# Optimization experiments

Hardware: AMD Instinct MI355X
Metric: run time of the kernel (lower is better)

## Reference

```python
import jax, jax.numpy as jnp
import numpy as np

B, N, C, H = 64, 4096, 128, 4
ALPHA = 0.2  # leaky_relu negative slope


def setup_inputs() -> dict:
    key = jax.random.key(0)
    k1, k2, k3, k4, k5 = jax.random.split(key, 5)
    V = jax.random.normal(k1, (B, N, C), dtype=jnp.float32)
    graph_size = jax.random.randint(k2, (B,), 1, N + 1, dtype=jnp.int32)
    # xavier_uniform-like init for weight [C, H*C] and tune_weight [1, H, C]
    lim_w = float(np.sqrt(6.0 / (C + H * C)))
    weight = jax.random.uniform(k3, (C, H * C), minval=-lim_w, maxval=lim_w, dtype=jnp.float32)
    lim_t = float(np.sqrt(6.0 / (H + C)))
    tune_weight = jax.random.uniform(k4, (1, H, C), minval=-lim_t, maxval=lim_t, dtype=jnp.float32)
    bias = jnp.full((H * C,), 0.01, dtype=jnp.float32)
    return {"V": V, "graph_size": graph_size, "weight": weight, "bias": bias, "tune_weight": tune_weight}


def reference(V, graph_size, weight, bias, tune_weight):
    # valid-node mask: node n of graph b is valid iff n < graph_size[b]
    mask = jnp.arange(N)[None, :] < graph_size[:, None]          # [B, N]
    # linear projection: [B, N, C] @ [C, H*C] + bias -> [B, N, H, C]
    Vg = (jnp.einsum('bnc,cd->bnd', V, weight) + bias).reshape(B, N, H, C)
    # attention logits per head: sum over features of tune_weight * Vg
    a = jnp.einsum('bnhc,ohc->bnh', Vg, tune_weight)             # [B, N, H]
    a = jnp.where(a >= 0, a, ALPHA * a)                          # leaky_relu
    # per-graph (segment) softmax over valid nodes
    a = jnp.where(mask[:, :, None], a, -jnp.inf)
    a = jax.nn.softmax(a, axis=1)                                # [B, N, H]
    # weighted segment sum -> [B, H, C] -> [B, H*C] (concat=True)
    out = jnp.einsum('bnhc,bnh->bhc', Vg, a)
    return out.reshape(B, H * C)
```

## Files before the change

### kernel.cpp

```cpp
#include <hip/hip_runtime.h>

#define NB 64
#define NN 4096
#define NC 128
#define NH 4
#define HC (NH * NC)
#define PSTRIDE (8 + HC)
#define NSLICE 16
#define LRELU 0.2f

__global__ __launch_bounds__(128) void k0_wt(const float* __restrict__ W,
                                             const float* __restrict__ bias,
                                             const float* __restrict__ tune,
                                             float* __restrict__ wtbt)
{
    const int bid = blockIdx.x;
    const int t = threadIdx.x;
    const float* src = (bid < NC) ? (W + (size_t)bid * HC) : bias;
    float* dst = (bid < NC) ? (wtbt + bid * NH) : (wtbt + NC * NH);
    const float4 a = reinterpret_cast<const float4*>(src)[t];
    const float4 b = reinterpret_cast<const float4*>(tune)[t];
    float p = a.x * b.x + a.y * b.y + a.z * b.z + a.w * b.w;
    #pragma unroll
    for (int off = 16; off; off >>= 1) p += __shfl_xor(p, off, 32);
    if ((t & 31) == 0) dst[t >> 5] = p;
}

__global__ __launch_bounds__(256, 4) void k1_part(const float* __restrict__ V,
                                                  const int* __restrict__ gs,
                                                  const float* __restrict__ wtbt,
                                                  float* __restrict__ part)
{
    const int slice = blockIdx.x;
    const int b = blockIdx.y;
    const int tid = threadIdx.x;
    const int hw = tid >> 5;
    const int lane = tid & 31;
    const int h = lane >> 3;
    const int j = lane & 7;
    const int w = slice * 8 + hw;
    const int gsz = gs[b];

    float wtk[16];
    #pragma unroll
    for (int u = 0; u < 16; ++u) wtk[u] = wtbt[(16 * j + u) * NH + h];
    const float bt = wtbt[HC + h];

    const int rem = gsz - w;
    const int iters = rem > 0 ? ((rem + 127) >> 7) : 0;

    float l = 0.f;
    float S[16] = {};

    const size_t STR = (size_t)128 * NC;
    const float* vp = V + ((size_t)b * NN + w) * NC + j * 16;

    float4 A0, A1, A2, A3, B0, B1, B2, B3;
    if (iters > 0) {
        A0 = reinterpret_cast<const float4*>(vp)[0];
        A1 = reinterpret_cast<const float4*>(vp)[1];
        A2 = reinterpret_cast<const float4*>(vp)[2];
        A3 = reinterpret_cast<const float4*>(vp)[3];
        const float* p1 = vp + (iters > 1 ? STR : 0);
        B0 = reinterpret_cast<const float4*>(p1)[0];
        B1 = reinterpret_cast<const float4*>(p1)[1];
        B2 = reinterpret_cast<const float4*>(p1)[2];
        B3 = reinterpret_cast<const float4*>(p1)[3];
    }
    for (int i = 0; i < iters; ++i) {
        const float* p2 = vp + (i + 2 < iters ? 2 * STR : 0);
        const float4 C0 = reinterpret_cast<const float4*>(p2)[0];
        const float4 C1 = reinterpret_cast<const float4*>(p2)[1];
        const float4 C2 = reinterpret_cast<const float4*>(p2)[2];
        const float4 C3 = reinterpret_cast<const float4*>(p2)[3];
        vp += STR;

        float a0 = A0.x * wtk[0]  + A0.y * wtk[1]  + A0.z * wtk[2]  + A0.w * wtk[3];
        float a1 = A1.x * wtk[4]  + A1.y * wtk[5]  + A1.z * wtk[6]  + A1.w * wtk[7];
        float a2 = A2.x * wtk[8]  + A2.y * wtk[9]  + A2.z * wtk[10] + A2.w * wtk[11];
        float a3 = A3.x * wtk[12] + A3.y * wtk[13] + A3.z * wtk[14] + A3.w * wtk[15];
        float lg = (a0 + a1) + (a2 + a3);
        lg += __shfl_xor(lg, 1, 32);
        lg += __shfl_xor(lg, 2, 32);
        lg += __shfl_xor(lg, 4, 32);
        float x = lg + bt;
        x = (x >= 0.f) ? x : LRELU * x;
        const float p = __expf(x);
        l += p;
        S[0]  += p * A0.x;  S[1]  += p * A0.y;  S[2]  += p * A0.z;  S[3]  += p * A0.w;
        S[4]  += p * A1.x;  S[5]  += p * A1.y;  S[6]  += p * A1.z;  S[7]  += p * A1.w;
        S[8]  += p * A2.x;  S[9]  += p * A2.y;  S[10] += p * A2.z;  S[11] += p * A2.w;
        S[12] += p * A3.x;  S[13] += p * A3.y;  S[14] += p * A3.z;  S[15] += p * A3.w;
        A0 = B0; A1 = B1; A2 = B2; A3 = B3;
        B0 = C0; B1 = C1; B2 = C2; B3 = C3;
    }

    __shared__ float llds[8][4];
    __shared__ float Sall[8][4][132];
    if (j == 0) llds[hw][h] = l;
    #pragma unroll
    for (int t = 0; t < 4; ++t) {
        float4 s4;
        s4.x = S[4 * t]; s4.y = S[4 * t + 1]; s4.z = S[4 * t + 2]; s4.w = S[4 * t + 3];
        *reinterpret_cast<float4*>(&Sall[hw][h][16 * j + 4 * t]) = s4;
    }
    __syncthreads();
    float* pb = part + (size_t)(b * NSLICE + slice) * PSTRIDE;
    if (tid < 4) {
        pb[tid] = 0.f;
        float L = 0.f;
        #pragma unroll
        for (int ww = 0; ww < 8; ++ww) L += llds[ww][tid];
        pb[4 + tid] = L;
    }
    #pragma unroll
    for (int r = 0; r < 2; ++r) {
        const int e = tid + r * 256;
        const int hh = e >> 7, k = e & 127;
        float s = 0.f;
        #pragma unroll
        for (int ww = 0; ww < 8; ++ww) s += Sall[ww][hh][k];
        pb[8 + e] = s;
    }
}

__global__ __launch_bounds__(128) void k2_out(const float* __restrict__ part,
                                              const float* __restrict__ W,
                                              const float* __restrict__ bias,
                                              float* __restrict__ out)
{
    const int b = blockIdx.x;
    const int h = blockIdx.y;
    const int tid = threadIdx.x;
    const float* pb = part + (size_t)b * NSLICE * PSTRIDE;

    __shared__ float Sn[NC];
    __shared__ float sL;
    if (tid == 0) {
        float L = 0.f;
        #pragma unroll
        for (int c = 0; c < NSLICE; ++c) L += pb[(size_t)c * PSTRIDE + 4 + h];
        sL = L;
    }
    __syncthreads();
    {
        float s = 0.f;
        #pragma unroll 4
        for (int c = 0; c < NSLICE; ++c)
            s += pb[(size_t)c * PSTRIDE + 8 + h * NC + tid];
        Sn[tid] = s / sL;
    }
    __syncthreads();
    const int d = h * NC + tid;
    float acc = 0.f;
    #pragma unroll 4
    for (int k = 0; k < NC; ++k) acc += Sn[k] * W[(size_t)k * HC + d];
    out[(size_t)b * HC + d] = acc + bias[d];
}

extern "C" void kernel_launch(void* const* d_in, const int* in_sizes, int n_in,
                              void* d_out, int out_size, void* d_ws, size_t ws_size,
                              hipStream_t stream)
{
    const float* V    = (const float*)d_in[0];
    const int*   gsz  = (const int*)d_in[1];
    const float* W    = (const float*)d_in[2];
    const float* bias = (const float*)d_in[3];
    const float* tune = (const float*)d_in[4];
    float* out  = (float*)d_out;
    float* wtbt = (float*)d_ws;
    float* part = wtbt + PSTRIDE;

    hipLaunchKernelGGL(k0_wt, dim3(NC + 1), dim3(128), 0, stream, W, bias, tune, wtbt);
    hipLaunchKernelGGL(k1_part, dim3(NSLICE, NB), dim3(256), 0, stream, V, gsz, wtbt, part);
    hipLaunchKernelGGL(k2_out, dim3(NB, NH), dim3(128), 0, stream, part, W, bias, out);
}
```

Measured before the change: 49.58 us.

## Fuse final reduction and output projection into partial kernel via last-block atomic counter

Removes the separate output kernel: each slice block writes its partials, fences, and atomically bumps a per-graph counter. The last block for a graph merges all slices, normalises and does the 128x512 projection. k0 now zeroes the counters each call. This saves a kernel launch and its dependency gap, at the cost of an atomic, fences, and a serial tail of work done by one block per graph.

Measured after the change: 180.2 us. 263% more time.

```diff
diff --git a/kernel.cpp b/kernel.cpp
--- a/kernel.cpp
+++ b/kernel.cpp
@@ -9,6 +9,7 @@
 #define NSLICE 16
 #define LRELU 0.2f
 
+
 __global__ __launch_bounds__(128) void k0_wt(const float* __restrict__ W,
                                              const float* __restrict__ bias,
                                              const float* __restrict__ tune,
@@ -16,6 +17,9 @@
 {
     const int bid = blockIdx.x;
     const int t = threadIdx.x;
+    if (bid == NC && t < 64) {
+        reinterpret_cast<int*>(wtbt + PSTRIDE)[t] = 0;
+    }
     const float* src = (bid < NC) ? (W + (size_t)bid * HC) : bias;
     float* dst = (bid < NC) ? (wtbt + bid * NH) : (wtbt + NC * NH);
     const float4 a = reinterpret_cast<const float4*>(src)[t];
@@ -26,11 +30,17 @@
     if ((t & 31) == 0) dst[t >> 5] = p;
 }
 
-__global__ __launch_bounds__(256, 4) void k1_part(const float* __restrict__ V,
-                                                  const int* __restrict__ gs,
-                                                  const float* __restrict__ wtbt,
-                                                  float* __restrict__ part)
+__global__ __launch_bounds__(256, 4) void k1_fused(const float* __restrict__ V,
+                                                   const int* __restrict__ gs,
+                                                   float* __restrict__ ws,
+                                                   const float* __restrict__ W,
+                                                   const float* __restrict__ bias,
+                                                   float* __restrict__ out)
 {
+    const float* wtbt = ws;
+    int* cnt = reinterpret_cast<int*>(ws + PSTRIDE);
+    float* part = ws + PSTRIDE + 64;
+
     const int slice = blockIdx.x;
     const int b = blockIdx.y;
     const int tid = threadIdx.x;
@@ -97,6 +107,9 @@
 
     __shared__ float llds[8][4];
     __shared__ float Sall[8][4][132];
+    __shared__ float sLh[4];
+    __shared__ float MrgSn[HC];
+    __shared__ int   sOld;
     if (j == 0) llds[hw][h] = l;
     #pragma unroll
     for (int t = 0; t < 4; ++t) {
@@ -107,7 +120,6 @@
     __syncthreads();
     float* pb = part + (size_t)(b * NSLICE + slice) * PSTRIDE;
     if (tid < 4) {
-        pb[tid] = 0.f;
         float L = 0.f;
         #pragma unroll
         for (int ww = 0; ww < 8; ++ww) L += llds[ww][tid];
@@ -122,40 +134,40 @@
         for (int ww = 0; ww < 8; ++ww) s += Sall[ww][hh][k];
         pb[8 + e] = s;
     }
-}
 
-__global__ __launch_bounds__(128) void k2_out(const float* __restrict__ part,
-                                              const float* __restrict__ W,
-                                              const float* __restrict__ bias,
-                                              float* __restrict__ out)
-{
-    const int b = blockIdx.x;
-    const int h = blockIdx.y;
-    const int tid = threadIdx.x;
-    const float* pb = part + (size_t)b * NSLICE * PSTRIDE;
+    __threadfence();
+    __syncthreads();
+    if (tid == 0) sOld = atomicAdd(&cnt[b], 1);
+    __syncthreads();
+    if (sOld != NSLICE - 1) return;
+    __threadfence();
 
-    __shared__ float Sn[NC];
-    __shared__ float sL;
-    if (tid == 0) {
+    const float* pg = part + (size_t)b * NSLICE * PSTRIDE;
+    if (tid < 4) {
         float L = 0.f;
         #pragma unroll
-        for (int c = 0; c < NSLICE; ++c) L += pb[(size_t)c * PSTRIDE + 4 + h];
-        sL = L;
+        for (int c = 0; c < NSLICE; ++c) L += pg[(size_t)c * PSTRIDE + 4 + tid];
+        sLh[tid] = L;
     }
     __syncthreads();
-    {
+    #pragma unroll
+    for (int r = 0; r < 2; ++r) {
+        const int e = tid + r * 256;
         float s = 0.f;
         #pragma unroll 4
-        for (int c = 0; c < NSLICE; ++c)
-            s += pb[(size_t)c * PSTRIDE + 8 + h * NC + tid];
-        Sn[tid] = s / sL;
+        for (int c = 0; c < NSLICE; ++c) s += pg[(size_t)c * PSTRIDE + 8 + e];
+        MrgSn[e] = s / sLh[e >> 7];
     }
     __syncthreads();
-    const int d = h * NC + tid;
-    float acc = 0.f;
-    #pragma unroll 4
-    for (int k = 0; k < NC; ++k) acc += Sn[k] * W[(size_t)k * HC + d];
-    out[(size_t)b * HC + d] = acc + bias[d];
+    #pragma unroll
+    for (int r = 0; r < 2; ++r) {
+        const int d = tid + r * 256;
+        const int hh = d >> 7;
+        float acc = 0.f;
+        #pragma unroll 4
+        for (int k = 0; k < NC; ++k) acc += MrgSn[hh * NC + k] * W[(size_t)k * HC + d];
+        out[(size_t)b * HC + d] = acc + bias[d];
+    }
 }
 
 extern "C" void kernel_launch(void* const* d_in, const int* in_sizes, int n_in,
@@ -167,11 +179,9 @@
     const float* W    = (const float*)d_in[2];
     const float* bias = (const float*)d_in[3];
     const float* tune = (const float*)d_in[4];
-    float* out  = (float*)d_out;
-    float* wtbt = (float*)d_ws;
-    float* part = wtbt + PSTRIDE;
+    float* out = (float*)d_out;
+    float* ws  = (float*)d_ws;
 
-    hipLaunchKernelGGL(k0_wt, dim3(NC + 1), dim3(128), 0, stream, W, bias, tune, wtbt);
-    hipLaunchKernelGGL(k1_part, dim3(NSLICE, NB), dim3(256), 0, stream, V, gsz, wtbt, part);
-    hipLaunchKernelGGL(k2_out, dim3(NB, NH), dim3(128), 0, stream, part, W, bias, out);
+    hipLaunchKernelGGL(k0_wt, dim3(NC + 1), dim3(128), 0, stream, W, bias, tune, ws);
+    hipLaunchKernelGGL(k1_fused, dim3(NSLICE, NB), dim3(256), 0, stream, V, gsz, ws, W, bias, out);
 }
```

## Double slices and interleave two row streams per warp; merge heads in output kernel

Applied to the files above, without the earlier changes.

Raises the number of node slices per graph so more blocks run concurrently. Each warp now processes two independent rows per iteration, one 256 rows further on, with their loads and shuffle reductions interleaved to raise memory-level parallelism. The final kernel handles all four heads in one 256-thread block per graph. The cost is more partial sums to reduce and a larger register footprint per thread.

New measurement: 66.51 us. 1.34x slower.

```diff
diff --git a/kernel.cpp b/kernel.cpp
--- a/kernel.cpp
+++ b/kernel.cpp
@@ -6,7 +6,7 @@
 #define NH 4
 #define HC (NH * NC)
 #define PSTRIDE (8 + HC)
-#define NSLICE 16
+#define NSLICE 32
 #define LRELU 0.2f
 
 __global__ __launch_bounds__(128) void k0_wt(const float* __restrict__ W,
@@ -47,52 +47,73 @@
     const float bt = wtbt[HC + h];
 
     const int rem = gsz - w;
-    const int iters = rem > 0 ? ((rem + 127) >> 7) : 0;
+    const int iters = rem > 0 ? ((rem + 255) >> 8) : 0;
+    const int npair = (iters + 1) >> 1;
 
     float l = 0.f;
     float S[16] = {};
 
-    const size_t STR = (size_t)128 * NC;
-    const float* vp = V + ((size_t)b * NN + w) * NC + j * 16;
-
-    float4 A0, A1, A2, A3, B0, B1, B2, B3;
-    if (iters > 0) {
-        A0 = reinterpret_cast<const float4*>(vp)[0];
-        A1 = reinterpret_cast<const float4*>(vp)[1];
-        A2 = reinterpret_cast<const float4*>(vp)[2];
-        A3 = reinterpret_cast<const float4*>(vp)[3];
-        const float* p1 = vp + (iters > 1 ? STR : 0);
-        B0 = reinterpret_cast<const float4*>(p1)[0];
-        B1 = reinterpret_cast<const float4*>(p1)[1];
-        B2 = reinterpret_cast<const float4*>(p1)[2];
-        B3 = reinterpret_cast<const float4*>(p1)[3];
-    }
-    for (int i = 0; i < iters; ++i) {
-        const float* p2 = vp + (i + 2 < iters ? 2 * STR : 0);
-        const float4 C0 = reinterpret_cast<const float4*>(p2)[0];
-        const float4 C1 = reinterpret_cast<const float4*>(p2)[1];
-        const float4 C2 = reinterpret_cast<const float4*>(p2)[2];
-        const float4 C3 = reinterpret_cast<const float4*>(p2)[3];
-        vp += STR;
-
-        float a0 = A0.x * wtk[0]  + A0.y * wtk[1]  + A0.z * wtk[2]  + A0.w * wtk[3];
-        float a1 = A1.x * wtk[4]  + A1.y * wtk[5]  + A1.z * wtk[6]  + A1.w * wtk[7];
-        float a2 = A2.x * wtk[8]  + A2.y * wtk[9]  + A2.z * wtk[10] + A2.w * wtk[11];
-        float a3 = A3.x * wtk[12] + A3.y * wtk[13] + A3.z * wtk[14] + A3.w * wtk[15];
-        float lg = (a0 + a1) + (a2 + a3);
-        lg += __shfl_xor(lg, 1, 32);
-        lg += __shfl_xor(lg, 2, 32);
-        lg += __shfl_xor(lg, 4, 32);
-        float x = lg + bt;
-        x = (x >= 0.f) ? x : LRELU * x;
-        const float p = __expf(x);
-        l += p;
-        S[0]  += p * A0.x;  S[1]  += p * A0.y;  S[2]  += p * A0.z;  S[3]  += p * A0.w;
-        S[4]  += p * A1.x;  S[5]  += p * A1.y;  S[6]  += p * A1.z;  S[7]  += p * A1.w;
-        S[8]  += p * A2.x;  S[9]  += p * A2.y;  S[10] += p * A2.z;  S[11] += p * A2.w;
-        S[12] += p * A3.x;  S[13] += p * A3.y;  S[14] += p * A3.z;  S[15] += p * A3.w;
-        A0 = B0; A1 = B1; A2 = B2; A3 = B3;
-        B0 = C0; B1 = C1; B2 = C2; B3 = C3;
+    const size_t RSTR = (size_t)256 * NC;
+
+    const float* r0p = V + ((size_t)b * NN + w) * NC + j * 16;
+    const float* r1p = r0p + (iters > 1 ? RSTR : 0);
+
+    float4 A0, A1, A2, A3, D0, D1, D2, D3;
+    if (npair > 0) {
+        A0 = reinterpret_cast<const float4*>(r0p)[0];
+        A1 = reinterpret_cast<const float4*>(r0p)[1];
+        A2 = reinterpret_cast<const float4*>(r0p)[2];
+        A3 = reinterpret_cast<const float4*>(r0p)[3];
+        D0 = reinterpret_cast<const float4*>(r1p)[0];
+        D1 = reinterpret_cast<const float4*>(r1p)[1];
+        D2 = reinterpret_cast<const float4*>(r1p)[2];
+        D3 = reinterpret_cast<const float4*>(r1p)[3];
+    }
+    for (int t = 0; t < npair; ++t) {
+        const float* n0 = r0p + ((2 * t + 2 < iters) ? 2 * RSTR : 0);
+        const float* n1 = r1p + ((2 * t + 3 < iters) ? 2 * RSTR : 0);
+        const float4 N0 = reinterpret_cast<const float4*>(n0)[0];
+        const float4 N1 = reinterpret_cast<const float4*>(n0)[1];
+        const float4 N2 = reinterpret_cast<const float4*>(n0)[2];
+        const float4 N3 = reinterpret_cast<const float4*>(n0)[3];
+        const float4 M0 = reinterpret_cast<const float4*>(n1)[0];
+        const float4 M1 = reinterpret_cast<const float4*>(n1)[1];
+        const float4 M2 = reinterpret_cast<const float4*>(n1)[2];
+        const float4 M3 = reinterpret_cast<const float4*>(n1)[3];
+
+        float g0 = A0.x * wtk[0]  + A0.y * wtk[1]  + A0.z * wtk[2]  + A0.w * wtk[3]
+                 + A1.x * wtk[4]  + A1.y * wtk[5]  + A1.z * wtk[6]  + A1.w * wtk[7]
+                 + A2.x * wtk[8]  + A2.y * wtk[9]  + A2.z * wtk[10] + A2.w * wtk[11]
+                 + A3.x * wtk[12] + A3.y * wtk[13] + A3.z * wtk[14] + A3.w * wtk[15];
+        float g1 = D0.x * wtk[0]  + D0.y * wtk[1]  + D0.z * wtk[2]  + D0.w * wtk[3]
+                 + D1.x * wtk[4]  + D1.y * wtk[5]  + D1.z * wtk[6]  + D1.w * wtk[7]
+                 + D2.x * wtk[8]  + D2.y * wtk[9]  + D2.z * wtk[10] + D2.w * wtk[11]
+                 + D3.x * wtk[12] + D3.y * wtk[13] + D3.z * wtk[14] + D3.w * wtk[15];
+        g0 += __shfl_xor(g0, 1, 32);
+        g1 += __shfl_xor(g1, 1, 32);
+        g0 += __shfl_xor(g0, 2, 32);
+        g1 += __shfl_xor(g1, 2, 32);
+        g0 += __shfl_xor(g0, 4, 32);
+        g1 += __shfl_xor(g1, 4, 32);
+        float x0 = g0 + bt;
+        float x1 = g1 + bt;
+        x0 = (x0 >= 0.f) ? x0 : LRELU * x0;
+        x1 = (x1 >= 0.f) ? x1 : LRELU * x1;
+        float p0 = __expf(x0);
+        float p1 = __expf(x1);
+        p1 = (2 * t + 1 < iters) ? p1 : 0.f;
+        l += p0 + p1;
+        S[0]  += p0 * A0.x + p1 * D0.x;  S[1]  += p0 * A0.y + p1 * D0.y;
+        S[2]  += p0 * A0.z + p1 * D0.z;  S[3]  += p0 * A0.w + p1 * D0.w;
+        S[4]  += p0 * A1.x + p1 * D1.x;  S[5]  += p0 * A1.y + p1 * D1.y;
+        S[6]  += p0 * A1.z + p1 * D1.z;  S[7]  += p0 * A1.w + p1 * D1.w;
+        S[8]  += p0 * A2.x + p1 * D2.x;  S[9]  += p0 * A2.y + p1 * D2.y;
+        S[10] += p0 * A2.z + p1 * D2.z;  S[11] += p0 * A2.w + p1 * D2.w;
+        S[12] += p0 * A3.x + p1 * D3.x;  S[13] += p0 * A3.y + p1 * D3.y;
+        S[14] += p0 * A3.z + p1 * D3.z;  S[15] += p0 * A3.w + p1 * D3.w;
+        A0 = N0; A1 = N1; A2 = N2; A3 = N3;
+        D0 = M0; D1 = M1; D2 = M2; D3 = M3;
+        r0p = n0; r1p = n1;
     }
 
     __shared__ float llds[8][4];
@@ -107,7 +128,6 @@
     __syncthreads();
     float* pb = part + (size_t)(b * NSLICE + slice) * PSTRIDE;
     if (tid < 4) {
-        pb[tid] = 0.f;
         float L = 0.f;
         #pragma unroll
         for (int ww = 0; ww < 8; ++ww) L += llds[ww][tid];
@@ -124,38 +144,42 @@
     }
 }
 
-__global__ __launch_bounds__(128) void k2_out(const float* __restrict__ part,
+__global__ __launch_bounds__(256) void k2_out(const float* __restrict__ part,
                                               const float* __restrict__ W,
                                               const float* __restrict__ bias,
                                               float* __restrict__ out)
 {
     const int b = blockIdx.x;
-    const int h = blockIdx.y;
     const int tid = threadIdx.x;
     const float* pb = part + (size_t)b * NSLICE * PSTRIDE;
 
-    __shared__ float Sn[NC];
-    __shared__ float sL;
-    if (tid == 0) {
+    __shared__ float Lh[4];
+    __shared__ float Sn[HC];
+    if (tid < 4) {
         float L = 0.f;
         #pragma unroll
-        for (int c = 0; c < NSLICE; ++c) L += pb[(size_t)c * PSTRIDE + 4 + h];
-        sL = L;
+        for (int c = 0; c < NSLICE; ++c) L += pb[(size_t)c * PSTRIDE + 4 + tid];
+        Lh[tid] = L;
     }
     __syncthreads();
-    {
+    #pragma unroll
+    for (int r = 0; r < 2; ++r) {
+        const int e = tid + r * 256;
         float s = 0.f;
+        #pragma unroll 8
+        for (int c = 0; c < NSLICE; ++c) s += pb[(size_t)c * PSTRIDE + 8 + e];
+        Sn[e] = s / Lh[e >> 7];
+    }
+    __syncthreads();
+    #pragma unroll
+    for (int r = 0; r < 2; ++r) {
+        const int d = tid + r * 256;
+        const int hh = d >> 7;
+        float acc = 0.f;
         #pragma unroll 4
-        for (int c = 0; c < NSLICE; ++c)
-            s += pb[(size_t)c * PSTRIDE + 8 + h * NC + tid];
-        Sn[tid] = s / sL;
-    }
-    __syncthreads();
-    const int d = h * NC + tid;
-    float acc = 0.f;
-    #pragma unroll 4
-    for (int k = 0; k < NC; ++k) acc += Sn[k] * W[(size_t)k * HC + d];
-    out[(size_t)b * HC + d] = acc + bias[d];
+        for (int k = 0; k < NC; ++k) acc += Sn[hh * NC + k] * W[(size_t)k * HC + d];
+        out[(size_t)b * HC + d] = acc + bias[d];
+    }
 }
 
 extern "C" void kernel_launch(void* const* d_in, const int* in_sizes, int n_in,
@@ -173,5 +197,5 @@
 
     hipLaunchKernelGGL(k0_wt, dim3(NC + 1), dim3(128), 0, stream, W, bias, tune, wtbt);
     hipLaunchKernelGGL(k1_part, dim3(NSLICE, NB), dim3(256), 0, stream, V, gsz, wtbt, part);
-    hipLaunchKernelGGL(k2_out, dim3(NB, NH), dim3(128), 0, stream, part, W, bias, out);
-}
+    hipLaunchKernelGGL(k2_out, dim3(NB), dim3(256), 0, stream, part, W, bias, out);
+}
```
